# Kernel tuning notes

Hardware: AMD Instinct MI355X
Metric: run time of the kernel (lower is better)

## Reference

```python
import jax, jax.numpy as jnp
import numpy as np

NUM_HEADS = 16
EMB_DIM = 1024
HEAD_DIM = EMB_DIM // NUM_HEADS


def setup_inputs() -> dict:
    key = jax.random.key(0)
    k1, k2, k3, k4 = jax.random.split(key, 4)
    B, S = 2, 2048
    X = jax.random.normal(k1, (B, S, EMB_DIM), dtype=jnp.float32)
    # torch Linear(in, out, bias=False): y = x @ W.T ; store as [in, out]
    Wq = jax.random.normal(k2, (EMB_DIM, EMB_DIM), dtype=jnp.float32) * (EMB_DIM ** -0.5)
    Wk = jax.random.normal(k3, (EMB_DIM, HEAD_DIM), dtype=jnp.float32) * (EMB_DIM ** -0.5)
    Wv = jax.random.normal(k4, (EMB_DIM, HEAD_DIM), dtype=jnp.float32) * (EMB_DIM ** -0.5)
    return {"X": X, "Wq": Wq, "Wk": Wk, "Wv": Wv}


def reference(X, Wq, Wk, Wv):
    B, S, E = X.shape
    H, D = NUM_HEADS, HEAD_DIM
    q = (X @ Wq).reshape(B, S, H, D).transpose(0, 2, 1, 3)  # [B,H,S,D]
    k = X @ Wk  # [B,S,D] shared K head
    v = X @ Wv  # [B,S,D] shared V head
    scores = jnp.einsum('bhsd,btd->bhst', q, k) / jnp.sqrt(jnp.float32(D))
    causal = jnp.tril(jnp.ones((S, S), dtype=bool))
    scores = jnp.where(causal, scores, -jnp.inf)
    probs = jax.nn.softmax(scores, axis=-1)  # [B,H,S,S]
    out = jnp.einsum('bhst,btd->bhsd', probs, v)  # [B,H,S,D]
    return out.transpose(0, 2, 1, 3).reshape(B, S, E)
```

## Files before the change

### kernel.cpp

```cpp
#include <hip/hip_runtime.h>
#include <stdint.h>

#define NH   16
#define EMB  1024
#define HD   64
#define BSZ  2
#define SEQ  2048
#define NROW (BSZ * SEQ)

typedef __attribute__((ext_vector_type(8))) short bf16x8;
typedef __attribute__((ext_vector_type(4))) float f32x4;

__device__ __forceinline__ uint16_t f2bf(float f) {
    union { float f; uint32_t i; } v; v.f = f;
    uint32_t r = v.i + 0x7FFFu + ((v.i >> 16) & 1u);
    return (uint16_t)(r >> 16);
}
__device__ __forceinline__ uint32_t pack2(float a, float b) {
    return (uint32_t)f2bf(a) | ((uint32_t)f2bf(b) << 16);
}
__device__ __forceinline__ uint32_t cvtpk(float a, float b) {
    uint32_t r;
    asm("v_cvt_pk_bf16_f32 %0, %1, %2" : "=v"(r) : "v"(a), "v"(b));
    return r;
}

__device__ __forceinline__ void gl2lds16(const uint16_t* g, uint16_t* l) {
    __builtin_amdgcn_global_load_lds(
        static_cast<const uint32_t*>(static_cast<const void*>(g)),
        static_cast<uint32_t*>(static_cast<void*>(l)), 16, 0, 0);
}

__global__ __launch_bounds__(256) void prep_w(
    const float* __restrict__ Wq, const float* __restrict__ Wk,
    const float* __restrict__ Wv, uint16_t* __restrict__ Wqt,
    uint16_t* __restrict__ Wkt, uint16_t* __restrict__ Wvt)
{
    __shared__ uint16_t T[64][72];
    const int tid = threadIdx.x;
    const int id = blockIdx.x;
    const float* W; uint16_t* Wt; int k0, n0, ldw;
    if (id < 256)      { W = Wq; Wt = Wqt; k0 = (id >> 4) * 64; n0 = (id & 15) * 64; ldw = EMB; }
    else if (id < 272) { W = Wk; Wt = Wkt; k0 = (id - 256) * 64; n0 = 0; ldw = HD; }
    else               { W = Wv; Wt = Wvt; k0 = (id - 272) * 64; n0 = 0; ldw = HD; }

    const int r = tid >> 2, c4 = (tid & 3) * 16;
#pragma unroll
    for (int i = 0; i < 4; ++i) {
        float4 wv = *(const float4*)&W[(size_t)(k0 + r) * ldw + n0 + c4 + 4 * i];
        T[r][c4 + 4 * i + 0] = f2bf(wv.x); T[r][c4 + 4 * i + 1] = f2bf(wv.y);
        T[r][c4 + 4 * i + 2] = f2bf(wv.z); T[r][c4 + 4 * i + 3] = f2bf(wv.w);
    }
    __syncthreads();
    const int n = tid >> 2, kk = (tid & 3) * 16;
    uint32_t o[8];
#pragma unroll
    for (int i = 0; i < 8; ++i)
        o[i] = (uint32_t)T[kk + 2 * i][n] | ((uint32_t)T[kk + 2 * i + 1][n] << 16);
    uint16_t* dst = &Wt[(size_t)(n0 + n) * EMB + k0 + kk];
    *(uint4*)dst       = make_uint4(o[0], o[1], o[2], o[3]);
    *(uint4*)(dst + 8) = make_uint4(o[4], o[5], o[6], o[7]);
}

__global__ __launch_bounds__(256) void qkv_gemm_mfma6(
    const float* __restrict__ X, const uint16_t* __restrict__ Wqt,
    const uint16_t* __restrict__ Wkt, const uint16_t* __restrict__ Wvt,
    float* __restrict__ Qout, uint16_t* __restrict__ Kbf,
    uint16_t* __restrict__ Vtbf)
{
    const int tid  = threadIdx.x;
    const int w    = tid >> 6, lane = tid & 63;
    const int l    = lane & 15, quad = lane >> 4;
    const int wm   = w & 1, wn = w >> 1;
    const int nt   = blockIdx.x;
    const int m0   = blockIdx.y * 64;

    __shared__ uint16_t As[2][64 * 64];
    __shared__ uint16_t Bs[2][128 * 64];

    const float* gAx[2]; uint32_t ldsA[2];
#pragma unroll
    for (int i = 0; i < 2; ++i) {
        int G = (w * 2 + i) * 64 + lane;
        int r = G >> 3, cg = (G & 7) ^ (r & 7);
        gAx[i] = &X[(size_t)(m0 + r) * EMB + cg * 8];
        ldsA[i] = (uint32_t)G * 8;
    }
    const uint16_t* gB[4]; uint32_t ldsB[4];
#pragma unroll
    for (int i = 0; i < 4; ++i) {
        int G = (w * 4 + i) * 64 + lane;
        int r = G >> 3, cg = (G & 7) ^ (r & 7);
        const uint16_t* bs;
        if (nt < 8)      bs = &Wqt[(size_t)(nt * 128 + r) * EMB + cg * 8];
        else if (r < 64) bs = &Wkt[(size_t)r * EMB + cg * 8];
        else             bs = &Wvt[(size_t)(r - 64) * EMB + cg * 8];
        gB[i] = bs;
        ldsB[i] = (w * 4 + i) * 512;
    }

    uint32_t offA[2][2], offB[4][2];
#pragma unroll
    for (int i = 0; i < 2; ++i)
#pragma unroll
        for (int kh = 0; kh < 2; ++kh) {
            int row = 32 * wm + 16 * i + l;
            offA[i][kh] = row * 64 + (((kh * 4 + quad) ^ (row & 7)) * 8);
        }
#pragma unroll
    for (int j = 0; j < 4; ++j)
#pragma unroll
        for (int kh = 0; kh < 2; ++kh) {
            int row = 64 * wn + 16 * j + l;
            offB[j][kh] = row * 64 + (((kh * 4 + quad) ^ (row & 7)) * 8);
        }

    f32x4 acc[2][4] = {};

    float4 a0[2], a1[2];
#pragma unroll
    for (int i = 0; i < 2; ++i) {
        a0[i] = *(const float4*)gAx[i];
        a1[i] = *(const float4*)(gAx[i] + 4);
        gAx[i] += 64;
    }
#pragma unroll
    for (int i = 0; i < 4; ++i) { gl2lds16(gB[i], &Bs[0][ldsB[i]]); gB[i] += 64; }
#pragma unroll
    for (int i = 0; i < 2; ++i)
        *(uint4*)&As[0][ldsA[i]] =
            make_uint4(cvtpk(a0[i].x, a0[i].y), cvtpk(a0[i].z, a0[i].w),
                       cvtpk(a1[i].x, a1[i].y), cvtpk(a1[i].z, a1[i].w));
    __syncthreads();

    for (int ks = 0; ks < 16; ++ks) {
        const int cur = ks & 1, nxt = cur ^ 1;
        if (ks < 15) {
#pragma unroll
            for (int i = 0; i < 2; ++i) {
                a0[i] = *(const float4*)gAx[i];
                a1[i] = *(const float4*)(gAx[i] + 4);
                gAx[i] += 64;
            }
#pragma unroll
            for (int i = 0; i < 4; ++i) { gl2lds16(gB[i], &Bs[nxt][ldsB[i]]); gB[i] += 64; }
        }
#pragma unroll
        for (int kh = 0; kh < 2; ++kh) {
            bf16x8 af[2], bfr[4];
#pragma unroll
            for (int i = 0; i < 2; ++i) af[i] = *(const bf16x8*)&As[cur][offA[i][kh]];
#pragma unroll
            for (int j = 0; j < 4; ++j) bfr[j] = *(const bf16x8*)&Bs[cur][offB[j][kh]];
#pragma unroll
            for (int i = 0; i < 2; ++i)
#pragma unroll
                for (int j = 0; j < 4; ++j)
                    acc[i][j] = __builtin_amdgcn_mfma_f32_16x16x32_bf16(
                        af[i], bfr[j], acc[i][j], 0, 0, 0);
        }
        if (ks < 15) {
#pragma unroll
            for (int i = 0; i < 2; ++i)
                *(uint4*)&As[nxt][ldsA[i]] =
                    make_uint4(cvtpk(a0[i].x, a0[i].y), cvtpk(a0[i].z, a0[i].w),
                               cvtpk(a1[i].x, a1[i].y), cvtpk(a1[i].z, a1[i].w));
        }
        __syncthreads();
    }

    if (nt < 8) {
#pragma unroll
        for (int i = 0; i < 2; ++i)
#pragma unroll
            for (int j = 0; j < 4; ++j)
#pragma unroll
                for (int r = 0; r < 4; ++r)
                    Qout[(size_t)(m0 + 32 * wm + 16 * i + 4 * quad + r) * EMB
                         + nt * 128 + 64 * wn + 16 * j + l] = acc[i][j][r];
    } else if (wn == 0) {
#pragma unroll
        for (int i = 0; i < 2; ++i)
#pragma unroll
            for (int j = 0; j < 4; ++j)
#pragma unroll
                for (int r = 0; r < 4; ++r)
                    Kbf[(size_t)(m0 + 32 * wm + 16 * i + 4 * quad + r) * HD
                        + 16 * j + l] = f2bf(acc[i][j][r]);
    } else {
#pragma unroll
        for (int i = 0; i < 2; ++i)
#pragma unroll
            for (int j = 0; j < 4; ++j)
#pragma unroll
                for (int r = 0; r < 4; ++r)
                    Vtbf[(size_t)(16 * j + l) * NROW
                         + m0 + 32 * wm + 16 * i + 4 * quad + r] = f2bf(acc[i][j][r]);
    }
}

__global__ __launch_bounds__(256) void mqa_attn(
    const uint16_t* __restrict__ Kbf, const uint16_t* __restrict__ Vtbf,
    float* __restrict__ Out)
{
    const int tid  = threadIdx.x;
    const int w    = tid >> 6;
    const int lane = tid & 63;
    const int l    = lane & 15;
    const int quad = lane >> 4;
    const int i  = blockIdx.x;
    const int h  = blockIdx.y, b = blockIdx.z;
    const int qt0 = 31 - i, qt1 = i;
    const int q00 = qt0 * 64, q01 = qt1 * 64;

    __shared__ __align__(16) uint16_t Ks[2][64 * 64];
    __shared__ __align__(16) uint16_t Vs[2][64 * 64];
    __shared__ __align__(16) uint16_t Ps[2][64][72];

    const float C = 0.125f * 1.4426950408889634f;
    const int sr = tid >> 2, sc = (tid & 3) * 16;

    const uint16_t* kSrc[2]; const uint16_t* vSrc[2]; uint32_t dstE[2];
#pragma unroll
    for (int i2 = 0; i2 < 2; ++i2) {
        int G = (w * 2 + i2) * 64 + lane;
        int r = G >> 3, g = G & 7;
        int pr = (r & 32) + ((r >> 2) & 3) * 8 + ((r & 16) >> 2) + (r & 3);
        int cg = g ^ (r & 7);
        kSrc[i2] = &Kbf[(size_t)(b * SEQ + pr) * HD + cg * 8];
        vSrc[i2] = &Vtbf[(size_t)r * NROW + b * SEQ + cg * 8];
        dstE[i2] = (uint32_t)(w * 2 + i2) * 512;
    }

#pragma unroll
    for (int i2 = 0; i2 < 2; ++i2) {
        gl2lds16(kSrc[i2], &Ks[0][dstE[i2]]);
        gl2lds16(vSrc[i2], &Vs[0][dstE[i2]]);
        kSrc[i2] += 64 * HD;
        vSrc[i2] += 64;
    }

#pragma unroll
    for (int t = 0; t < 2; ++t) {
        const int q0t = t ? q01 : q00;
        const float* src = &Out[(size_t)(b * SEQ + q0t + sr) * EMB + h * HD + sc];
        float4 f0 = *(const float4*)(src + 0);
        float4 f1 = *(const float4*)(src + 4);
        float4 f2 = *(const float4*)(src + 8);
        float4 f3 = *(const float4*)(src + 12);
        *(uint4*)&Ps[t][sr][sc] =
            make_uint4(pack2(f0.x * C, f0.y * C), pack2(f0.z * C, f0.w * C),
                       pack2(f1.x * C, f1.y * C), pack2(f1.z * C, f1.w * C));
        *(uint4*)&Ps[t][sr][sc + 8] =
            make_uint4(pack2(f2.x * C, f2.y * C), pack2(f2.z * C, f2.w * C),
                       pack2(f3.x * C, f3.y * C), pack2(f3.z * C, f3.w * C));
    }
    __syncthreads();

    bf16x8 qf[2][2];
#pragma unroll
    for (int t = 0; t < 2; ++t) {
        qf[t][0] = *(const bf16x8*)&Ps[t][16 * w + l][quad * 8];
        qf[t][1] = *(const bf16x8*)&Ps[t][16 * w + l][32 + quad * 8];
    }

    uint32_t off[4][2];
#pragma unroll
    for (int ts = 0; ts < 4; ++ts)
#pragma unroll
        for (int kh = 0; kh < 2; ++kh)
            off[ts][kh] = (16 * ts + l) * 64 + (((4 * kh + quad) ^ (l & 7)) * 8);

    bf16x8 ones;
#pragma unroll
    for (int j = 0; j < 8; ++j) ones[j] = (short)0x3F80;

    f32x4 accO[2][4] = {};
    f32x4 accSum[2] = {};
    const int qi_l = 16 * w + l;

    auto body = [&](int kb, bool DO1, bool M0, bool M1) __attribute__((always_inline)) {
        const int cur = kb & 1, nxt = cur ^ 1;

        bf16x8 ka[4][2], vb[4][2];
#pragma unroll
        for (int ts = 0; ts < 4; ++ts) {
            ka[ts][0] = *(const bf16x8*)&Ks[cur][off[ts][0]];
            ka[ts][1] = *(const bf16x8*)&Ks[cur][off[ts][1]];
            vb[ts][0] = *(const bf16x8*)&Vs[cur][off[ts][0]];
            vb[ts][1] = *(const bf16x8*)&Vs[cur][off[ts][1]];
        }

        if (kb < qt0) {
#pragma unroll
            for (int i2 = 0; i2 < 2; ++i2) {
                gl2lds16(kSrc[i2], &Ks[nxt][dstE[i2]]);
                gl2lds16(vSrc[i2], &Vs[nxt][dstE[i2]]);
                kSrc[i2] += 64 * HD;
                vSrc[i2] += 64;
            }
        }

        f32x4 accS0[4] = {}, accS1[4] = {};
#pragma unroll
        for (int ts = 0; ts < 4; ++ts) {
            accS0[ts] = __builtin_amdgcn_mfma_f32_16x16x32_bf16(ka[ts][0], qf[0][0], accS0[ts], 0, 0, 0);
            accS0[ts] = __builtin_amdgcn_mfma_f32_16x16x32_bf16(ka[ts][1], qf[0][1], accS0[ts], 0, 0, 0);
        }
        if (DO1) {
#pragma unroll
            for (int ts = 0; ts < 4; ++ts) {
                accS1[ts] = __builtin_amdgcn_mfma_f32_16x16x32_bf16(ka[ts][0], qf[1][0], accS1[ts], 0, 0, 0);
                accS1[ts] = __builtin_amdgcn_mfma_f32_16x16x32_bf16(ka[ts][1], qf[1][1], accS1[ts], 0, 0, 0);
            }
        }

        {
            float pv[16];
#pragma unroll
            for (int ts = 0; ts < 4; ++ts)
#pragma unroll
                for (int r = 0; r < 4; ++r)
                    pv[4 * ts + r] = exp2f(accS0[ts][r]);
            if (M0) {
#pragma unroll
                for (int ts = 0; ts < 4; ++ts)
#pragma unroll
                    for (int r = 0; r < 4; ++r)
                        if ((((ts & 2) << 4) + ((ts & 1) << 2) + 8 * quad + r) > qi_l)
                            pv[4 * ts + r] = 0.f;
            }
            union { uint32_t u[4]; bf16x8 v; } A0, A1;
#pragma unroll
            for (int j = 0; j < 4; ++j) A0.u[j] = cvtpk(pv[2 * j],     pv[2 * j + 1]);
#pragma unroll
            for (int j = 0; j < 4; ++j) A1.u[j] = cvtpk(pv[8 + 2 * j], pv[9 + 2 * j]);
#pragma unroll
            for (int tn = 0; tn < 4; ++tn) {
                accO[0][tn] = __builtin_amdgcn_mfma_f32_16x16x32_bf16(A0.v, vb[tn][0], accO[0][tn], 0, 0, 0);
                accO[0][tn] = __builtin_amdgcn_mfma_f32_16x16x32_bf16(A1.v, vb[tn][1], accO[0][tn], 0, 0, 0);
            }
            accSum[0] = __builtin_amdgcn_mfma_f32_16x16x32_bf16(A0.v, ones, accSum[0], 0, 0, 0);
            accSum[0] = __builtin_amdgcn_mfma_f32_16x16x32_bf16(A1.v, ones, accSum[0], 0, 0, 0);
        }
        if (DO1) {
            float pv[16];
#pragma unroll
            for (int ts = 0; ts < 4; ++ts)
#pragma unroll
                for (int r = 0; r < 4; ++r)
                    pv[4 * ts + r] = exp2f(accS1[ts][r]);
            if (M1) {
#pragma unroll
                for (int ts = 0; ts < 4; ++ts)
#pragma unroll
                    for (int r = 0; r < 4; ++r)
                        if ((((ts & 2) << 4) + ((ts & 1) << 2) + 8 * quad + r) > qi_l)
                            pv[4 * ts + r] = 0.f;
            }
            union { uint32_t u[4]; bf16x8 v; } A0, A1;
#pragma unroll
            for (int j = 0; j < 4; ++j) A0.u[j] = cvtpk(pv[2 * j],     pv[2 * j + 1]);
#pragma unroll
            for (int j = 0; j < 4; ++j) A1.u[j] = cvtpk(pv[8 + 2 * j], pv[9 + 2 * j]);
#pragma unroll
            for (int tn = 0; tn < 4; ++tn) {
                accO[1][tn] = __builtin_amdgcn_mfma_f32_16x16x32_bf16(A0.v, vb[tn][0], accO[1][tn], 0, 0, 0);
                accO[1][tn] = __builtin_amdgcn_mfma_f32_16x16x32_bf16(A1.v, vb[tn][1], accO[1][tn], 0, 0, 0);
            }
            accSum[1] = __builtin_amdgcn_mfma_f32_16x16x32_bf16(A0.v, ones, accSum[1], 0, 0, 0);
            accSum[1] = __builtin_amdgcn_mfma_f32_16x16x32_bf16(A1.v, ones, accSum[1], 0, 0, 0);
        }

        if (kb < qt0) __syncthreads();
    };

    for (int kb = 0; kb < qt1; ++kb) body(kb, true,  false, false);
    body(qt1, true,  false, true);
    for (int kb = qt1 + 1; kb < qt0; ++kb) body(kb, false, false, false);
    body(qt0, false, true,  false);

#pragma unroll
    for (int t = 0; t < 2; ++t) {
        const int q0t = t ? q01 : q00;
#pragma unroll
        for (int r = 0; r < 4; ++r) {
            float invr = 1.0f / accSum[t][r];
            const int row = q0t + 16 * w + 4 * quad + r;
#pragma unroll
            for (int tn = 0; tn < 4; ++tn)
                Out[(size_t)(b * SEQ + row) * EMB + h * HD + 16 * tn + l] =
                    accO[t][tn][r] * invr;
        }
    }
}

__global__ __launch_bounds__(256) void qkv_gemm_vec(
    const float* __restrict__ X,  const float* __restrict__ Wq,
    const float* __restrict__ Wk, const float* __restrict__ Wv,
    float* __restrict__ Qout, uint16_t* __restrict__ Kbf,
    uint16_t* __restrict__ Vtbf)
{
    const int tid = threadIdx.x;
    const int tx = tid & 15, ty = tid >> 4;
    const int bx = blockIdx.x;
    const int m0 = blockIdx.y * 64;

    const float* W; int ldw, n0;
    if (bx < 16)       { W = Wq; ldw = EMB; n0 = bx * 64; }
    else if (bx == 16) { W = Wk; ldw = HD;  n0 = 0; }
    else               { W = Wv; ldw = HD;  n0 = 0; }

    __shared__ float sA[64][17];
    __shared__ float sB[16][64];

    float acc[4][4] = {};
    const int arow = tid >> 2, acol = (tid & 3) * 4;
    const int brow = tid >> 4, bcol = (tid & 15) * 4;

    for (int k0 = 0; k0 < EMB; k0 += 16) {
        float4 fa = *(const float4*)&X[(size_t)(m0 + arow) * EMB + k0 + acol];
        float4 fb = *(const float4*)&W[(size_t)(k0 + brow) * ldw + n0 + bcol];
        sA[arow][acol + 0] = fa.x; sA[arow][acol + 1] = fa.y;
        sA[arow][acol + 2] = fa.z; sA[arow][acol + 3] = fa.w;
        sB[brow][bcol + 0] = fb.x; sB[brow][bcol + 1] = fb.y;
        sB[brow][bcol + 2] = fb.z; sB[brow][bcol + 3] = fb.w;
        __syncthreads();
#pragma unroll
        for (int kk = 0; kk < 16; ++kk) {
            float a0 = sA[4 * ty + 0][kk];
            float a1 = sA[4 * ty + 1][kk];
            float a2 = sA[4 * ty + 2][kk];
            float a3 = sA[4 * ty + 3][kk];
            float4 bq = *(const float4*)&sB[kk][4 * tx];
            acc[0][0] += a0 * bq.x; acc[0][1] += a0 * bq.y; acc[0][2] += a0 * bq.z; acc[0][3] += a0 * bq.w;
            acc[1][0] += a1 * bq.x; acc[1][1] += a1 * bq.y; acc[1][2] += a1 * bq.z; acc[1][3] += a1 * bq.w;
            acc[2][0] += a2 * bq.x; acc[2][1] += a2 * bq.y; acc[2][2] += a2 * bq.z; acc[2][3] += a2 * bq.w;
            acc[3][0] += a3 * bq.x; acc[3][1] += a3 * bq.y; acc[3][2] += a3 * bq.z; acc[3][3] += a3 * bq.w;
        }
        __syncthreads();
    }

    if (bx < 16) {
#pragma unroll
        for (int i = 0; i < 4; ++i)
            *(float4*)&Qout[(size_t)(m0 + 4 * ty + i) * EMB + n0 + 4 * tx] =
                make_float4(acc[i][0], acc[i][1], acc[i][2], acc[i][3]);
    } else if (bx == 16) {
#pragma unroll
        for (int i = 0; i < 4; ++i) {
            ushort4 u; u.x = f2bf(acc[i][0]); u.y = f2bf(acc[i][1]);
            u.z = f2bf(acc[i][2]); u.w = f2bf(acc[i][3]);
            *(ushort4*)&Kbf[(size_t)(m0 + 4 * ty + i) * HD + 4 * tx] = u;
        }
    } else {
#pragma unroll
        for (int j = 0; j < 4; ++j) {
            ushort4 u; u.x = f2bf(acc[0][j]); u.y = f2bf(acc[1][j]);
            u.z = f2bf(acc[2][j]); u.w = f2bf(acc[3][j]);
            *(ushort4*)&Vtbf[(size_t)(4 * tx + j) * NROW + m0 + 4 * ty] = u;
        }
    }
}

extern "C" void kernel_launch(void* const* d_in, const int* in_sizes, int n_in,
                              void* d_out, int out_size, void* d_ws, size_t ws_size,
                              hipStream_t stream) {
    const float* X  = (const float*)d_in[0];
    const float* Wq = (const float*)d_in[1];
    const float* Wk = (const float*)d_in[2];
    const float* Wv = (const float*)d_in[3];
    float* OutP = (float*)d_out;

    char* ws = (char*)d_ws;
    const size_t MB = 1024 * 1024;
    const size_t KB = 1024;
    uint16_t* Wqt  = (uint16_t*)(ws);
    uint16_t* Wkt  = (uint16_t*)(ws + 2 * MB);
    uint16_t* Wvt  = (uint16_t*)(ws + 2 * MB + 128 * KB);
    uint16_t* Kbf  = (uint16_t*)(ws + 2 * MB + 256 * KB);
    uint16_t* Vtbf = (uint16_t*)(ws + 2 * MB + 768 * KB);

    if (ws_size >= 4 * MB) {
        prep_w<<<288, 256, 0, stream>>>(Wq, Wk, Wv, Wqt, Wkt, Wvt);
        qkv_gemm_mfma6<<<dim3(9, 64), 256, 0, stream>>>(X, Wqt, Wkt, Wvt,
                                                        OutP, Kbf, Vtbf);
        mqa_attn<<<dim3(16, NH, BSZ), 256, 0, stream>>>(Kbf, Vtbf, OutP);
    } else {
        uint16_t* KbfS  = (uint16_t*)d_ws;
        uint16_t* VtbfS = KbfS + (size_t)NROW * HD;
        qkv_gemm_vec<<<dim3(18, 64), 256, 0, stream>>>(X, Wq, Wk, Wv, OutP, KbfS, VtbfS);
        mqa_attn<<<dim3(16, NH, BSZ), 256, 0, stream>>>(KbfS, VtbfS, OutP);
    }
}
```

Measured before the change: 138.0 us.

## Split paired causal query tiles into one tile per block with larger grid

The attention kernel used to process two complementary query tiles (i and 31-i) per block so the causal work per block was balanced. Now each block handles a single 64-row query tile, and the grid doubles to 32 tiles per head. The Q staging buffer is dropped by reusing the K shared buffer for the swizzled Q load, which cuts shared memory, and a launch-bounds occupancy hint of 4 is added. The aim is more blocks and higher occupancy. The cost is uneven per-block work across the causal triangle, and K/V tiles are now read once per query tile instead of being shared by two.

```diff
diff --git a/kernel.cpp b/kernel.cpp
--- a/kernel.cpp
+++ b/kernel.cpp
@@ -199,7 +199,7 @@
     }
 }
 
-__global__ __launch_bounds__(256) void mqa_attn(
+__global__ __launch_bounds__(256, 4) void mqa_attn(
     const uint16_t* __restrict__ Kbf, const uint16_t* __restrict__ Vtbf,
     float* __restrict__ Out)
 {
@@ -208,14 +208,12 @@
     const int lane = tid & 63;
     const int l    = lane & 15;
     const int quad = lane >> 4;
-    const int i  = blockIdx.x;
     const int h  = blockIdx.y, b = blockIdx.z;
-    const int qt0 = 31 - i, qt1 = i;
-    const int q00 = qt0 * 64, q01 = qt1 * 64;
-
-    __shared__ __align__(16) uint16_t Ks[2][64 * 64];
-    __shared__ __align__(16) uint16_t Vs[2][64 * 64];
-    __shared__ __align__(16) uint16_t Ps[2][64][72];
+    const int qt = 31 - blockIdx.x;
+    const int q0 = qt * 64;
+
+    __shared__ __align__(16) uint16_t Ks[2][4096];
+    __shared__ __align__(16) uint16_t Vs[2][4096];
 
     const float C = 0.125f * 1.4426950408889634f;
     const int sr = tid >> 2, sc = (tid & 3) * 16;
@@ -232,6 +230,30 @@
         dstE[i2] = (uint32_t)(w * 2 + i2) * 512;
     }
 
+    {
+        const float* src = &Out[(size_t)(b * SEQ + q0 + sr) * EMB + h * HD + sc];
+        float4 f0 = *(const float4*)(src + 0);
+        float4 f1 = *(const float4*)(src + 4);
+        float4 f2 = *(const float4*)(src + 8);
+        float4 f3 = *(const float4*)(src + 12);
+        const int g0 = sc >> 3;
+        *(uint4*)&Ks[0][sr * 64 + ((g0 ^ (sr & 7)) * 8)] =
+            make_uint4(pack2(f0.x * C, f0.y * C), pack2(f0.z * C, f0.w * C),
+                       pack2(f1.x * C, f1.y * C), pack2(f1.z * C, f1.w * C));
+        *(uint4*)&Ks[0][sr * 64 + (((g0 + 1) ^ (sr & 7)) * 8)] =
+            make_uint4(pack2(f2.x * C, f2.y * C), pack2(f2.z * C, f2.w * C),
+                       pack2(f3.x * C, f3.y * C), pack2(f3.z * C, f3.w * C));
+    }
+    __syncthreads();
+
+    bf16x8 qf[2];
+    {
+        const int row = 16 * w + l;
+        qf[0] = *(const bf16x8*)&Ks[0][row * 64 + (((0 + quad) ^ (row & 7)) * 8)];
+        qf[1] = *(const bf16x8*)&Ks[0][row * 64 + (((4 + quad) ^ (row & 7)) * 8)];
+    }
+    __syncthreads();
+
 #pragma unroll
     for (int i2 = 0; i2 < 2; ++i2) {
         gl2lds16(kSrc[i2], &Ks[0][dstE[i2]]);
@@ -239,30 +261,7 @@
         kSrc[i2] += 64 * HD;
         vSrc[i2] += 64;
     }
-
-#pragma unroll
-    for (int t = 0; t < 2; ++t) {
-        const int q0t = t ? q01 : q00;
-        const float* src = &Out[(size_t)(b * SEQ + q0t + sr) * EMB + h * HD + sc];
-        float4 f0 = *(const float4*)(src + 0);
-        float4 f1 = *(const float4*)(src + 4);
-        float4 f2 = *(const float4*)(src + 8);
-        float4 f3 = *(const float4*)(src + 12);
-        *(uint4*)&Ps[t][sr][sc] =
-            make_uint4(pack2(f0.x * C, f0.y * C), pack2(f0.z * C, f0.w * C),
-                       pack2(f1.x * C, f1.y * C), pack2(f1.z * C, f1.w * C));
-        *(uint4*)&Ps[t][sr][sc + 8] =
-            make_uint4(pack2(f2.x * C, f2.y * C), pack2(f2.z * C, f2.w * C),
-                       pack2(f3.x * C, f3.y * C), pack2(f3.z * C, f3.w * C));
-    }
     __syncthreads();
-
-    bf16x8 qf[2][2];
-#pragma unroll
-    for (int t = 0; t < 2; ++t) {
-        qf[t][0] = *(const bf16x8*)&Ps[t][16 * w + l][quad * 8];
-        qf[t][1] = *(const bf16x8*)&Ps[t][16 * w + l][32 + quad * 8];
-    }
 
     uint32_t off[4][2];
 #pragma unroll
@@ -275,11 +274,11 @@
 #pragma unroll
     for (int j = 0; j < 8; ++j) ones[j] = (short)0x3F80;
 
-    f32x4 accO[2][4] = {};
-    f32x4 accSum[2] = {};
+    f32x4 accO[4] = {};
+    f32x4 accSum = {};
     const int qi_l = 16 * w + l;
 
-    auto body = [&](int kb, bool DO1, bool M0, bool M1) __attribute__((always_inline)) {
+    auto body = [&](int kb, bool M) __attribute__((always_inline)) {
         const int cur = kb & 1, nxt = cur ^ 1;
 
         bf16x8 ka[4][2], vb[4][2];
@@ -291,7 +290,7 @@
             vb[ts][1] = *(const bf16x8*)&Vs[cur][off[ts][1]];
         }
 
-        if (kb < qt0) {
+        if (kb < qt) {
 #pragma unroll
             for (int i2 = 0; i2 < 2; ++i2) {
                 gl2lds16(kSrc[i2], &Ks[nxt][dstE[i2]]);
@@ -301,97 +300,55 @@
             }
         }
 
-        f32x4 accS0[4] = {}, accS1[4] = {};
+        f32x4 accS[4] = {};
 #pragma unroll
         for (int ts = 0; ts < 4; ++ts) {
-            accS0[ts] = __builtin_amdgcn_mfma_f32_16x16x32_bf16(ka[ts][0], qf[0][0], accS0[ts], 0, 0, 0);
-            accS0[ts] = __builtin_amdgcn_mfma_f32_16x16x32_bf16(ka[ts][1], qf[0][1], accS0[ts], 0, 0, 0);
-        }
-        if (DO1) {
-#pragma unroll
-            for (int ts = 0; ts < 4; ++ts) {
-                accS1[ts] = __builtin_amdgcn_mfma_f32_16x16x32_bf16(ka[ts][0], qf[1][0], accS1[ts], 0, 0, 0);
-                accS1[ts] = __builtin_amdgcn_mfma_f32_16x16x32_bf16(ka[ts][1], qf[1][1], accS1[ts], 0, 0, 0);
-            }
-        }
-
-        {
-            float pv[16];
+            accS[ts] = __builtin_amdgcn_mfma_f32_16x16x32_bf16(ka[ts][0], qf[0], accS[ts], 0, 0, 0);
+            accS[ts] = __builtin_amdgcn_mfma_f32_16x16x32_bf16(ka[ts][1], qf[1], accS[ts], 0, 0, 0);
+        }
+
+        float pv[16];
+#pragma unroll
+        for (int ts = 0; ts < 4; ++ts)
+#pragma unroll
+            for (int r = 0; r < 4; ++r)
+                pv[4 * ts + r] = exp2f(accS[ts][r]);
+        if (M) {
 #pragma unroll
             for (int ts = 0; ts < 4; ++ts)
 #pragma unroll
                 for (int r = 0; r < 4; ++r)
-                    pv[4 * ts + r] = exp2f(accS0[ts][r]);
-            if (M0) {
-#pragma unroll
-                for (int ts = 0; ts < 4; ++ts)
-#pragma unroll
-                    for (int r = 0; r < 4; ++r)
-                        if ((((ts & 2) << 4) + ((ts & 1) << 2) + 8 * quad + r) > qi_l)
-                            pv[4 * ts + r] = 0.f;
-            }
-            union { uint32_t u[4]; bf16x8 v; } A0, A1;
-#pragma unroll
-            for (int j = 0; j < 4; ++j) A0.u[j] = cvtpk(pv[2 * j],     pv[2 * j + 1]);
-#pragma unroll
-            for (int j = 0; j < 4; ++j) A1.u[j] = cvtpk(pv[8 + 2 * j], pv[9 + 2 * j]);
-#pragma unroll
-            for (int tn = 0; tn < 4; ++tn) {
-                accO[0][tn] = __builtin_amdgcn_mfma_f32_16x16x32_bf16(A0.v, vb[tn][0], accO[0][tn], 0, 0, 0);
-                accO[0][tn] = __builtin_amdgcn_mfma_f32_16x16x32_bf16(A1.v, vb[tn][1], accO[0][tn], 0, 0, 0);
-            }
-            accSum[0] = __builtin_amdgcn_mfma_f32_16x16x32_bf16(A0.v, ones, accSum[0], 0, 0, 0);
-            accSum[0] = __builtin_amdgcn_mfma_f32_16x16x32_bf16(A1.v, ones, accSum[0], 0, 0, 0);
-        }
-        if (DO1) {
-            float pv[16];
-#pragma unroll
-            for (int ts = 0; ts < 4; ++ts)
-#pragma unroll
-                for (int r = 0; r < 4; ++r)
-                    pv[4 * ts + r] = exp2f(accS1[ts][r]);
-            if (M1) {
-#pragma unroll
-                for (int ts = 0; ts < 4; ++ts)
-#pragma unroll
-                    for (int r = 0; r < 4; ++r)
-                        if ((((ts & 2) << 4) + ((ts & 1) << 2) + 8 * quad + r) > qi_l)
-                            pv[4 * ts + r] = 0.f;
-            }
-            union { uint32_t u[4]; bf16x8 v; } A0, A1;
-#pragma unroll
-            for (int j = 0; j < 4; ++j) A0.u[j] = cvtpk(pv[2 * j],     pv[2 * j + 1]);
-#pragma unroll
-            for (int j = 0; j < 4; ++j) A1.u[j] = cvtpk(pv[8 + 2 * j], pv[9 + 2 * j]);
-#pragma unroll
-            for (int tn = 0; tn < 4; ++tn) {
-                accO[1][tn] = __builtin_amdgcn_mfma_f32_16x16x32_bf16(A0.v, vb[tn][0], accO[1][tn], 0, 0, 0);
-                accO[1][tn] = __builtin_amdgcn_mfma_f32_16x16x32_bf16(A1.v, vb[tn][1], accO[1][tn], 0, 0, 0);
-            }
-            accSum[1] = __builtin_amdgcn_mfma_f32_16x16x32_bf16(A0.v, ones, accSum[1], 0, 0, 0);
-            accSum[1] = __builtin_amdgcn_mfma_f32_16x16x32_bf16(A1.v, ones, accSum[1], 0, 0, 0);
-        }
-
-        if (kb < qt0) __syncthreads();
+                    if ((((ts & 2) << 4) + ((ts & 1) << 2) + 8 * quad + r) > qi_l)
+                        pv[4 * ts + r] = 0.f;
+        }
+        union { uint32_t u[4]; bf16x8 v; } A0, A1;
+#pragma unroll
+        for (int j = 0; j < 4; ++j) A0.u[j] = cvtpk(pv[2 * j],     pv[2 * j + 1]);
+#pragma unroll
+        for (int j = 0; j < 4; ++j) A1.u[j] = cvtpk(pv[8 + 2 * j], pv[9 + 2 * j]);
+
+#pragma unroll
+        for (int tn = 0; tn < 4; ++tn) {
+            accO[tn] = __builtin_amdgcn_mfma_f32_16x16x32_bf16(A0.v, vb[tn][0], accO[tn], 0, 0, 0);
+            accO[tn] = __builtin_amdgcn_mfma_f32_16x16x32_bf16(A1.v, vb[tn][1], accO[tn], 0, 0, 0);
+        }
+        accSum = __builtin_amdgcn_mfma_f32_16x16x32_bf16(A0.v, ones, accSum, 0, 0, 0);
+        accSum = __builtin_amdgcn_mfma_f32_16x16x32_bf16(A1.v, ones, accSum, 0, 0, 0);
+
+        if (kb < qt) __syncthreads();
     };
 
-    for (int kb = 0; kb < qt1; ++kb) body(kb, true,  false, false);
-    body(qt1, true,  false, true);
-    for (int kb = qt1 + 1; kb < qt0; ++kb) body(kb, false, false, false);
-    body(qt0, false, true,  false);
-
-#pragma unroll
-    for (int t = 0; t < 2; ++t) {
-        const int q0t = t ? q01 : q00;
-#pragma unroll
-        for (int r = 0; r < 4; ++r) {
-            float invr = 1.0f / accSum[t][r];
-            const int row = q0t + 16 * w + 4 * quad + r;
-#pragma unroll
-            for (int tn = 0; tn < 4; ++tn)
-                Out[(size_t)(b * SEQ + row) * EMB + h * HD + 16 * tn + l] =
-                    accO[t][tn][r] * invr;
-        }
+    for (int kb = 0; kb < qt; ++kb) body(kb, false);
+    body(qt, true);
+
+#pragma unroll
+    for (int r = 0; r < 4; ++r) {
+        float invr = 1.0f / accSum[r];
+        const int row = q0 + 16 * w + 4 * quad + r;
+#pragma unroll
+        for (int tn = 0; tn < 4; ++tn)
+            Out[(size_t)(b * SEQ + row) * EMB + h * HD + 16 * tn + l] =
+                accO[tn][r] * invr;
     }
 }
 
@@ -485,11 +442,11 @@
         prep_w<<<288, 256, 0, stream>>>(Wq, Wk, Wv, Wqt, Wkt, Wvt);
         qkv_gemm_mfma6<<<dim3(9, 64), 256, 0, stream>>>(X, Wqt, Wkt, Wvt,
                                                         OutP, Kbf, Vtbf);
-        mqa_attn<<<dim3(16, NH, BSZ), 256, 0, stream>>>(Kbf, Vtbf, OutP);
+        mqa_attn<<<dim3(32, NH, BSZ), 256, 0, stream>>>(Kbf, Vtbf, OutP);
     } else {
         uint16_t* KbfS  = (uint16_t*)d_ws;
         uint16_t* VtbfS = KbfS + (size_t)NROW * HD;
         qkv_gemm_vec<<<dim3(18, 64), 256, 0, stream>>>(X, Wq, Wk, Wv, OutP, KbfS, VtbfS);
-        mqa_attn<<<dim3(16, NH, BSZ), 256, 0, stream>>>(KbfS, VtbfS, OutP);
-    }
-}
+        mqa_attn<<<dim3(32, NH, BSZ), 256, 0, stream>>>(KbfS, VtbfS, OutP);
+    }
+}
```

Result: slower. 151.9 us (+10.1%).
